# Performance work log

Hardware: AMD Instinct MI355X
Metric: run time of the kernel (lower is better)

The kernel has to match this reference:

```python
import jax, jax.numpy as jnp
import numpy as np

VOCAB = 50257
N_EMBD = 640
BLOCK = 256
B = 16


def setup_inputs() -> dict:
    key = jax.random.key(0)
    ks = jax.random.split(key, 8)
    std = 0.02
    return {
        "idx": jax.random.randint(ks[0], (B, BLOCK), 0, VOCAB, dtype=jnp.int64 if jax.config.jax_enable_x64 else jnp.int32),
        "w_embed": jax.random.normal(ks[1], (VOCAB, N_EMBD), jnp.float32) * std,
        "w_pos": jax.random.normal(ks[2], (BLOCK, N_EMBD), jnp.float32) * std,
        "wq": jax.random.normal(ks[3], (N_EMBD, N_EMBD), jnp.float32) * std,
        "wk": jax.random.normal(ks[4], (N_EMBD, N_EMBD), jnp.float32) * std,
        "wv": jax.random.normal(ks[5], (N_EMBD, N_EMBD), jnp.float32) * std,
        "w_out": jax.random.normal(ks[6], (VOCAB, N_EMBD), jnp.float32) * std,
        "b_out": jnp.zeros((VOCAB,), jnp.float32),
    }


def reference(idx, w_embed, w_pos, wq, wk, wv, w_out, b_out):
    # idx: (B, T) token ids. Dropout is identity (eval mode).
    Bt, T = idx.shape
    x = w_embed[idx] + w_pos[:T]                      # (B, T, D)
    q = jnp.einsum('btd,ed->bte', x, wq)              # torch Linear: x @ W.T
    k = jnp.einsum('btd,ed->bte', x, wk)
    v = jnp.einsum('btd,ed->bte', x, wv)
    scale = jnp.asarray(N_EMBD ** 0.5, x.dtype)
    scores = jnp.einsum('btd,bsd->bts', q, k) / scale  # (B, T, T)
    causal = jnp.triu(jnp.ones((T, T), bool), k=1)     # True above diagonal
    scores = jnp.where(causal, jnp.asarray(-jnp.inf, scores.dtype), scores)
    attn = jax.nn.softmax(scores, axis=-1)
    attn_out = jnp.einsum('bts,bsd->btd', attn, v)     # (B, T, D)
    logits = jnp.einsum('btd,vd->btv', attn_out, w_out) + b_out  # (B, T, V)
    return logits
```

## Files before the change

### kernel.cpp

```cpp
#include <hip/hip_runtime.h>
#include <hip/hip_bf16.h>
#include <stdint.h>

#define VOCAB 50257
#define VPAD  50304
#define DIM   640
#define SEQ   256
#define NBATCH 16
#define MROWS 4096

using bf16 = __hip_bfloat16;
typedef __attribute__((ext_vector_type(8))) short short8;
typedef __attribute__((ext_vector_type(4))) float f32x4;

__device__ __forceinline__ void gld_lds16(const void* g, void* l) {
  __builtin_amdgcn_global_load_lds(
      (const __attribute__((address_space(1))) void*)g,
      (__attribute__((address_space(3))) void*)l, 16, 0, 0);
}

__global__ void embed_kernel(const int* __restrict__ idx,
                             const float* __restrict__ we,
                             const float* __restrict__ wp,
                             bf16* __restrict__ xb) {
  int row = blockIdx.x;
  int t = row & (SEQ - 1);
  int tok = idx[row];
  const float* src = we + (long)tok * DIM;
  const float* pos = wp + (long)t * DIM;
  for (int d = threadIdx.x; d < DIM; d += blockDim.x)
    xb[(long)row * DIM + d] = __float2bfloat16(src[d] + pos[d]);
}

__global__ void conv_kernel(const float* __restrict__ src, bf16* __restrict__ dst,
                            long n_src, long n_dst) {
  long i = (long)blockIdx.x * blockDim.x + threadIdx.x;
  long stride = (long)gridDim.x * blockDim.x;
  for (; i < n_dst; i += stride)
    dst[i] = __float2bfloat16(i < n_src ? src[i] : 0.f);
}

__global__ void transpose_v(const bf16* __restrict__ v, bf16* __restrict__ vt) {
  long i = (long)blockIdx.x * blockDim.x + threadIdx.x;
  if (i >= (long)NBATCH * DIM * SEQ) return;
  int t = (int)(i & (SEQ - 1));
  long be = i >> 8;
  int e = (int)(be % DIM);
  int b = (int)(be / DIM);
  vt[i] = v[((long)b * SEQ + t) * DIM + e];
}

__global__ void softmax_kernel(const float* __restrict__ sc, bf16* __restrict__ p) {
  int wid = threadIdx.x >> 6, lane = threadIdx.x & 63;
  int row = blockIdx.x * 4 + wid;
  int t = row & (SEQ - 1);
  const float* srow = sc + (long)row * SEQ;
  const float rsc = 0.03952847075210474f;
  float v[4];
  float mx = -1e30f;
#pragma unroll
  for (int i = 0; i < 4; ++i) {
    int s = lane + 64 * i;
    v[i] = (s <= t) ? srow[s] * rsc : -1e30f;
    mx = fmaxf(mx, v[i]);
  }
#pragma unroll
  for (int off = 32; off; off >>= 1) mx = fmaxf(mx, __shfl_xor(mx, off, 64));
  float sum = 0.f;
#pragma unroll
  for (int i = 0; i < 4; ++i) {
    int s = lane + 64 * i;
    v[i] = (s <= t) ? __expf(v[i] - mx) : 0.f;
    sum += v[i];
  }
#pragma unroll
  for (int off = 32; off; off >>= 1) sum += __shfl_xor(sum, off, 64);
  float inv = 1.f / sum;
#pragma unroll
  for (int i = 0; i < 4; ++i)
    p[(long)row * SEQ + lane + 64 * i] = __float2bfloat16(v[i] * inv);
}

template <typename OUT_T, bool BIAS>
__global__ __launch_bounds__(256, 2) void gemm_bt(
    const bf16* __restrict__ Ag, const bf16* __restrict__ Bg,
    OUT_T* __restrict__ Cg, const float* __restrict__ bias,
    int K, int ldc, int Nstore, long sA, long sB, long sC) {
  __shared__ bf16 As[128 * 32];
  __shared__ bf16 Bs[128 * 32];
  const int tid = threadIdx.x;
  const int wv = tid >> 6, lane = tid & 63;
  const int tm = blockIdx.x * 128, tn = blockIdx.y * 128;
  const int bz = blockIdx.z;
  const bf16* A = Ag + (long)bz * sA + (long)tm * K;
  const bf16* B = Bg + (long)bz * sB + (long)tn * K;

  f32x4 acc[4][4] = {};
  const int wr = (wv >> 1) * 64, wc = (wv & 1) * 64;
  const int lr = lane & 15, lk = (lane >> 4) * 8;
  const int srow0 = wv * 32;
  const int g_r = lane >> 2, g_k = (lane & 3) * 8;

  for (int k0 = 0; k0 < K; k0 += 32) {
#pragma unroll
    for (int j = 0; j < 2; ++j) {
      int r = srow0 + j * 16;
      gld_lds16(A + (long)(r + g_r) * K + k0 + g_k, &As[r * 32]);
      gld_lds16(B + (long)(r + g_r) * K + k0 + g_k, &Bs[r * 32]);
    }
    __syncthreads();
    short8 a[4], b[4];
#pragma unroll
    for (int m = 0; m < 4; ++m)
      a[m] = *(const short8*)&As[(wr + m * 16 + lr) * 32 + lk];
#pragma unroll
    for (int n = 0; n < 4; ++n)
      b[n] = *(const short8*)&Bs[(wc + n * 16 + lr) * 32 + lk];
#pragma unroll
    for (int m = 0; m < 4; ++m)
#pragma unroll
      for (int n = 0; n < 4; ++n)
        acc[m][n] = __builtin_amdgcn_mfma_f32_16x16x32_bf16(a[m], b[n], acc[m][n], 0, 0, 0);
    __syncthreads();
  }

  OUT_T* C = Cg + (long)bz * sC;
  const int crow0 = tm + wr + (lane >> 4) * 4;
  const int ccol0 = tn + wc + (lane & 15);
#pragma unroll
  for (int m = 0; m < 4; ++m)
#pragma unroll
    for (int n = 0; n < 4; ++n) {
      int col = ccol0 + n * 16;
      if (col < Nstore) {
        float bv = BIAS ? bias[col] : 0.f;
#pragma unroll
        for (int j = 0; j < 4; ++j) {
          long row = crow0 + m * 16 + j;
          float val = acc[m][n][j] + bv;
          if constexpr (sizeof(OUT_T) == 2)
            C[row * ldc + col] = __float2bfloat16(val);
          else
            C[row * ldc + col] = val;
        }
      }
    }
}

extern "C" void kernel_launch(void* const* d_in, const int* in_sizes, int n_in,
                              void* d_out, int out_size, void* d_ws, size_t ws_size,
                              hipStream_t stream) {
  const int*   idx     = (const int*)d_in[0];
  const float* w_embed = (const float*)d_in[1];
  const float* w_pos   = (const float*)d_in[2];
  const float* wq      = (const float*)d_in[3];
  const float* wk      = (const float*)d_in[4];
  const float* wv      = (const float*)d_in[5];
  const float* w_out   = (const float*)d_in[6];
  const float* b_out   = (const float*)d_in[7];
  float* out = (float*)d_out;

  size_t off = 0;
  auto alloc = [&](size_t bytes) {
    void* p = (char*)d_ws + off;
    off += (bytes + 255) & ~(size_t)255;
    return p;
  };
  bf16* x_bf    = (bf16*)alloc((size_t)MROWS * DIM * 2);
  bf16* wqkv_bf = (bf16*)alloc((size_t)3 * DIM * DIM * 2);
  bf16* wout_bf = (bf16*)alloc((size_t)VPAD * DIM * 2);
  bf16* qkv     = (bf16*)alloc((size_t)3 * MROWS * DIM * 2);
  bf16* vT      = (bf16*)alloc((size_t)NBATCH * DIM * SEQ * 2);
  float* scores = (float*)alloc((size_t)NBATCH * SEQ * SEQ * 4);
  bf16* P       = (bf16*)alloc((size_t)NBATCH * SEQ * SEQ * 2);
  bf16* attn    = (bf16*)alloc((size_t)MROWS * DIM * 2);

  const long QKV_S = (long)MROWS * DIM;
  const long W_S   = (long)DIM * DIM;

  embed_kernel<<<MROWS, 256, 0, stream>>>(idx, w_embed, w_pos, x_bf);

  conv_kernel<<<512, 256, 0, stream>>>(wq, wqkv_bf,           W_S, W_S);
  conv_kernel<<<512, 256, 0, stream>>>(wk, wqkv_bf + W_S,     W_S, W_S);
  conv_kernel<<<512, 256, 0, stream>>>(wv, wqkv_bf + 2 * W_S, W_S, W_S);
  conv_kernel<<<4096, 256, 0, stream>>>(w_out, wout_bf, (long)VOCAB * DIM, (long)VPAD * DIM);

  gemm_bt<bf16, false><<<dim3(MROWS / 128, DIM / 128, 3), 256, 0, stream>>>(
      x_bf, wqkv_bf, qkv, nullptr, DIM, DIM, DIM, 0, W_S, QKV_S);

  {
    long n = (long)NBATCH * DIM * SEQ;
    transpose_v<<<(int)((n + 255) / 256), 256, 0, stream>>>(qkv + 2 * QKV_S, vT);
  }

  gemm_bt<float, false><<<dim3(SEQ / 128, SEQ / 128, NBATCH), 256, 0, stream>>>(
      qkv, qkv + QKV_S, scores, nullptr, DIM, SEQ, SEQ,
      (long)SEQ * DIM, (long)SEQ * DIM, (long)SEQ * SEQ);

  softmax_kernel<<<MROWS / 4, 256, 0, stream>>>(scores, P);

  gemm_bt<bf16, false><<<dim3(SEQ / 128, DIM / 128, NBATCH), 256, 0, stream>>>(
      P, vT, attn, nullptr, SEQ, DIM, DIM,
      (long)SEQ * SEQ, (long)DIM * SEQ, (long)SEQ * DIM);

  gemm_bt<float, true><<<dim3(MROWS / 128, VPAD / 128, 1), 256, 0, stream>>>(
      attn, wout_bf, out, b_out, DIM, VOCAB, VOCAB, 0, 0, 0);
}
```

Baseline: 625.9 us.

## Replace vocab projection GEMM with 256x256 double-buffered swizzled LDS kernel

```diff
diff --git a/kernel.cpp b/kernel.cpp
--- a/kernel.cpp
+++ b/kernel.cpp
@@ -3,11 +3,12 @@
 #include <stdint.h>
 
 #define VOCAB 50257
-#define VPAD  50304
+#define VPAD  50432
 #define DIM   640
 #define SEQ   256
 #define NBATCH 16
 #define MROWS 4096
+#define NTILES 10
 
 using bf16 = __hip_bfloat16;
 typedef __attribute__((ext_vector_type(8))) short short8;
@@ -18,6 +19,9 @@
       (const __attribute__((address_space(1))) void*)g,
       (__attribute__((address_space(3))) void*)l, 16, 0, 0);
 }
+
+#define BAR() asm volatile("s_barrier" ::: "memory")
+#define VMC(n) asm volatile("s_waitcnt vmcnt(" #n ")" ::: "memory")
 
 __global__ void embed_kernel(const int* __restrict__ idx,
                              const float* __restrict__ we,
@@ -143,6 +147,122 @@
           else
             C[row * ldc + col] = val;
         }
+      }
+    }
+}
+
+__global__ __launch_bounds__(512, 1) void gemm256(
+    const bf16* __restrict__ Ag, const bf16* __restrict__ Bg,
+    float* __restrict__ Cg, const float* __restrict__ bias) {
+  __shared__ __align__(16) char lds[131072];
+  const int tid = threadIdx.x;
+  const int lane = tid & 63, wv = tid >> 6;
+  const int wm = wv >> 2, wn = wv & 3;
+
+  int bid = blockIdx.x;
+  int swz = (bid & 7) * 394 + (bid >> 3);
+  const int tm = swz & 15, tn = swz >> 4;
+
+  int e0, e1, du0, du1;
+  {
+    int L0 = tid * 16;
+    int L1 = (512 + tid) * 16;
+    int Lp0 = L0 ^ (((L0 >> 9) & 1) << 5);
+    int Lp1 = L1 ^ (((L1 >> 9) & 1) << 5);
+    e0 = ((Lp0 >> 6) & 127) * DIM + ((Lp0 >> 13) & 1) * 32 + ((Lp0 & 63) >> 1);
+    e1 = ((Lp1 >> 6) & 127) * DIM + ((Lp1 >> 13) & 1) * 32 + ((Lp1 & 63) >> 1);
+    du0 = (wv << 6) * 16;
+    du1 = (512 + (wv << 6)) * 16;
+  }
+  auto STAGE = [&](int halfBase, const bf16* src) {
+    gld_lds16(src + e0, lds + halfBase + du0);
+    gld_lds16(src + e1, lds + halfBase + du1);
+  };
+
+  const bf16* Abase = Ag + (long)tm * 256 * DIM;
+  const bf16* Bbase = Bg + (long)tn * 256 * DIM;
+
+  const int lr = lane & 15, h16 = lane >> 4;
+  const int laneOff = (lr * 64 + h16 * 16) ^ ((lr & 8) << 2);
+  const int abase = wm * 16384 + laneOff;
+  const int bbase = 32768 + (wn >> 1) * 16384 + (wn & 1) * 4096 + laneOff;
+
+  f32x4 acc[8][4] = {};
+  short8 a0[2][4], a1[2][4], b[2][4];
+
+#define READ_A(DST, SLOT, MFB)                                                \
+  { _Pragma("unroll") for (int ks = 0; ks < 2; ++ks)                          \
+    _Pragma("unroll") for (int mf = 0; mf < 4; ++mf)                          \
+      DST[ks][mf] = *(const short8*)(lds + (SLOT) + abase + ks * 8192 +       \
+                                     ((MFB) + mf) * 1024); }
+#define READ_B(SLOT)                                                          \
+  { _Pragma("unroll") for (int ks = 0; ks < 2; ++ks)                          \
+    _Pragma("unroll") for (int nf = 0; nf < 4; ++nf)                          \
+      b[ks][nf] = *(const short8*)(lds + (SLOT) + bbase + ks * 8192 +         \
+                                   nf * 1024); }
+#define MFMA_G(AARR, KS, ROFF)                                                \
+  __builtin_amdgcn_s_setprio(1);                                              \
+  { _Pragma("unroll") for (int mf = 0; mf < 4; ++mf)                          \
+    _Pragma("unroll") for (int nf = 0; nf < 4; ++nf)                          \
+      acc[(ROFF) + mf][nf] = __builtin_amdgcn_mfma_f32_16x16x32_bf16(         \
+          AARR[KS][mf], b[KS][nf], acc[(ROFF) + mf][nf], 0, 0, 0); }          \
+  __builtin_amdgcn_s_setprio(0);
+
+  STAGE(0,             Abase);
+  STAGE(16384,         Abase + 128 * DIM);
+  STAGE(32768,         Bbase);
+  STAGE(49152,         Bbase + 128 * DIM);
+  STAGE(65536 + 32768, Bbase + 64);
+  STAGE(65536 + 0,     Abase + 64);
+  STAGE(65536 + 16384, Abase + 128 * DIM + 64);
+  VMC(6);
+  BAR();
+
+#pragma unroll
+  for (int T = 0; T < NTILES; ++T) {
+    const int slot = (T & 1) << 16;
+    const int nslot = ((T + 1) & 1) << 16;
+    READ_A(a0, slot, 0);
+    READ_B(slot);
+    if (T + 1 < NTILES) STAGE(nslot + 49152, Bbase + 128 * DIM + (T + 1) * 64);
+    BAR();
+    MFMA_G(a0, 0, 0);
+    BAR();
+    READ_A(a1, slot, 4);
+    if (T + 2 < NTILES) STAGE(slot + 32768, Bbase + (T + 2) * 64);
+    BAR();
+    MFMA_G(a0, 1, 0);
+    BAR();
+    if (T + 2 < NTILES) STAGE(slot + 0, Abase + (T + 2) * 64);
+    BAR();
+    MFMA_G(a1, 0, 4);
+    BAR();
+    if (T + 2 < NTILES) {
+      STAGE(slot + 16384, Abase + 128 * DIM + (T + 2) * 64);
+      VMC(6);
+    } else if (T + 1 < NTILES) {
+      VMC(0);
+    }
+    BAR();
+    MFMA_G(a1, 1, 4);
+    BAR();
+  }
+#undef READ_A
+#undef READ_B
+#undef MFMA_G
+
+  const int rowB = tm * 256 + wm * 128 + h16 * 4;
+  const int colB = tn * 256 + wn * 64 + lr;
+#pragma unroll
+  for (int mf = 0; mf < 8; ++mf)
+#pragma unroll
+    for (int nf = 0; nf < 4; ++nf) {
+      int col = colB + nf * 16;
+      if (col < VOCAB) {
+        float bv = bias[col];
+#pragma unroll
+        for (int jj = 0; jj < 4; ++jj)
+          Cg[(long)(rowB + mf * 16 + jj) * VOCAB + col] = acc[mf][nf][jj] + bv;
       }
     }
 }
@@ -203,6 +323,5 @@
       P, vT, attn, nullptr, SEQ, DIM, DIM,
       (long)SEQ * SEQ, (long)DIM * SEQ, (long)SEQ * DIM);
 
-  gemm_bt<float, true><<<dim3(MROWS / 128, VPAD / 128, 1), 256, 0, stream>>>(
-      attn, wout_bf, out, b_out, DIM, VOCAB, VOCAB, 0, 0, 0);
-}
+  gemm256<<<16 * 197, 512, 0, stream>>>(attn, wout_bf, out, b_out);
+}
```

New measurement: 652.5 us. 4.3% more time.

## Triple-buffer GEMM with swizzled LDS, XCD-aware tile remap, vectorized conversions

Applied to the files above, without the earlier changes.

```diff
diff --git a/kernel.cpp b/kernel.cpp
--- a/kernel.cpp
+++ b/kernel.cpp
@@ -3,7 +3,7 @@
 #include <stdint.h>
 
 #define VOCAB 50257
-#define VPAD  50304
+#define VPAD  50432
 #define DIM   640
 #define SEQ   256
 #define NBATCH 16
@@ -12,12 +12,16 @@
 using bf16 = __hip_bfloat16;
 typedef __attribute__((ext_vector_type(8))) short short8;
 typedef __attribute__((ext_vector_type(4))) float f32x4;
+struct bf16x4 { bf16 a, b, c, d; };
 
 __device__ __forceinline__ void gld_lds16(const void* g, void* l) {
   __builtin_amdgcn_global_load_lds(
       (const __attribute__((address_space(1))) void*)g,
       (__attribute__((address_space(3))) void*)l, 16, 0, 0);
 }
+
+#define BAR() asm volatile("s_barrier" ::: "memory")
+#define VMC(n) asm volatile("s_waitcnt vmcnt(" #n ")" ::: "memory")
 
 __global__ void embed_kernel(const int* __restrict__ idx,
                              const float* __restrict__ we,
@@ -28,16 +32,25 @@
   int tok = idx[row];
   const float* src = we + (long)tok * DIM;
   const float* pos = wp + (long)t * DIM;
-  for (int d = threadIdx.x; d < DIM; d += blockDim.x)
-    xb[(long)row * DIM + d] = __float2bfloat16(src[d] + pos[d]);
-}
-
-__global__ void conv_kernel(const float* __restrict__ src, bf16* __restrict__ dst,
-                            long n_src, long n_dst) {
-  long i = (long)blockIdx.x * blockDim.x + threadIdx.x;
-  long stride = (long)gridDim.x * blockDim.x;
-  for (; i < n_dst; i += stride)
-    dst[i] = __float2bfloat16(i < n_src ? src[i] : 0.f);
+  for (int d = threadIdx.x * 4; d < DIM; d += blockDim.x * 4) {
+    float4 s = *(const float4*)(src + d);
+    float4 p = *(const float4*)(pos + d);
+    bf16x4 o = { __float2bfloat16(s.x + p.x), __float2bfloat16(s.y + p.y),
+                 __float2bfloat16(s.z + p.z), __float2bfloat16(s.w + p.w) };
+    *(bf16x4*)(xb + (long)row * DIM + d) = o;
+  }
+}
+
+__global__ void conv4_kernel(const float* __restrict__ src, bf16* __restrict__ dst,
+                             long n_src, long n_dst) {
+  long i = ((long)blockIdx.x * blockDim.x + threadIdx.x) * 4;
+  long stride = (long)gridDim.x * blockDim.x * 4;
+  for (; i < n_dst; i += stride) {
+    float4 v = (i < n_src) ? *(const float4*)(src + i) : make_float4(0.f, 0.f, 0.f, 0.f);
+    bf16x4 o = { __float2bfloat16(v.x), __float2bfloat16(v.y),
+                 __float2bfloat16(v.z), __float2bfloat16(v.w) };
+    *(bf16x4*)(dst + i) = o;
+  }
 }
 
 __global__ void transpose_v(const bf16* __restrict__ v, bf16* __restrict__ vt) {
@@ -81,52 +94,86 @@
     p[(long)row * SEQ + lane + 64 * i] = __float2bfloat16(v[i] * inv);
 }
 
-template <typename OUT_T, bool BIAS>
-__global__ __launch_bounds__(256, 2) void gemm_bt(
+template <int NT, typename OUT_T, bool BIAS, bool SWZ>
+__global__ __launch_bounds__(256, 3) void gemm_pipe(
     const bf16* __restrict__ Ag, const bf16* __restrict__ Bg,
     OUT_T* __restrict__ Cg, const float* __restrict__ bias,
-    int K, int ldc, int Nstore, long sA, long sB, long sC) {
-  __shared__ bf16 As[128 * 32];
-  __shared__ bf16 Bs[128 * 32];
+    int K, int ldc, int Nstore, long sA, long sB, long sC,
+    int tmW, int chunk) {
+  __shared__ __align__(16) char lds[49152];
   const int tid = threadIdx.x;
-  const int wv = tid >> 6, lane = tid & 63;
-  const int tm = blockIdx.x * 128, tn = blockIdx.y * 128;
-  const int bz = blockIdx.z;
-  const bf16* A = Ag + (long)bz * sA + (long)tm * K;
-  const bf16* B = Bg + (long)bz * sB + (long)tn * K;
+  const int lane = tid & 63, wv = tid >> 6;
+  const int lr = lane & 15, h16 = lane >> 4;
+
+  int tm, tn, bz;
+  if constexpr (SWZ) {
+    int bid = blockIdx.x;
+    int s = (bid & 7) * chunk + (bid >> 3);
+    tm = s % tmW; tn = s / tmW; bz = 0;
+  } else {
+    tm = blockIdx.x; tn = blockIdx.y; bz = blockIdx.z;
+  }
+
+  const bf16* A = Ag + (long)bz * sA + (long)tm * 128 * K;
+  const bf16* B = Bg + (long)bz * sB + (long)tn * 128 * K;
+
+  int srcE[2], dstW[2];
+#pragma unroll
+  for (int j = 0; j < 2; ++j) {
+    int d = j * 256 + tid;
+    int b = d ^ ((d >> 3) & 3);
+    srcE[j] = (b >> 2) * K + (b & 3) * 8;
+    dstW[j] = (j * 256 + wv * 64) * 16;
+  }
+  auto STAGE = [&](int slot, int kOff) {
+#pragma unroll
+    for (int j = 0; j < 2; ++j) {
+      gld_lds16(A + srcE[j] + kOff, lds + slot + dstW[j]);
+      gld_lds16(B + srcE[j] + kOff, lds + slot + 8192 + dstW[j]);
+    }
+  };
+
+  const int wr = (wv >> 1) * 64, wc = (wv & 1) * 64;
+  int aoff[4], boff[4];
+#pragma unroll
+  for (int m = 0; m < 4; ++m) {
+    int La = (wr + m * 16 + lr) * 64 + h16 * 16;
+    aoff[m] = La ^ (((La >> 7) & 3) << 4);
+    int Lb = (wc + m * 16 + lr) * 64 + h16 * 16;
+    boff[m] = 8192 + (Lb ^ (((Lb >> 7) & 3) << 4));
+  }
 
   f32x4 acc[4][4] = {};
-  const int wr = (wv >> 1) * 64, wc = (wv & 1) * 64;
-  const int lr = lane & 15, lk = (lane >> 4) * 8;
-  const int srow0 = wv * 32;
-  const int g_r = lane >> 2, g_k = (lane & 3) * 8;
-
-  for (int k0 = 0; k0 < K; k0 += 32) {
-#pragma unroll
-    for (int j = 0; j < 2; ++j) {
-      int r = srow0 + j * 16;
-      gld_lds16(A + (long)(r + g_r) * K + k0 + g_k, &As[r * 32]);
-      gld_lds16(B + (long)(r + g_r) * K + k0 + g_k, &Bs[r * 32]);
-    }
-    __syncthreads();
-    short8 a[4], b[4];
-#pragma unroll
-    for (int m = 0; m < 4; ++m)
-      a[m] = *(const short8*)&As[(wr + m * 16 + lr) * 32 + lk];
-#pragma unroll
-    for (int n = 0; n < 4; ++n)
-      b[n] = *(const short8*)&Bs[(wc + n * 16 + lr) * 32 + lk];
+  short8 a[4], b[4];
+
+  STAGE(0, 0);
+  if (NT > 1) STAGE(16384, 32);
+  VMC(4);
+  BAR();
+
+#pragma unroll
+  for (int t = 0; t < NT; ++t) {
+    const int cur = (t % 3) * 16384;
+    if (t + 2 < NT) STAGE(((t + 2) % 3) * 16384, (t + 2) * 32);
+#pragma unroll
+    for (int m = 0; m < 4; ++m) a[m] = *(const short8*)(lds + cur + aoff[m]);
+#pragma unroll
+    for (int n = 0; n < 4; ++n) b[n] = *(const short8*)(lds + cur + boff[n]);
+    __builtin_amdgcn_s_setprio(1);
 #pragma unroll
     for (int m = 0; m < 4; ++m)
 #pragma unroll
       for (int n = 0; n < 4; ++n)
         acc[m][n] = __builtin_amdgcn_mfma_f32_16x16x32_bf16(a[m], b[n], acc[m][n], 0, 0, 0);
-    __syncthreads();
+    __builtin_amdgcn_s_setprio(0);
+    if (t + 2 < NT) { VMC(4); }
+    else if (t + 1 < NT) { VMC(0); }
+    BAR();
   }
 
   OUT_T* C = Cg + (long)bz * sC;
-  const int crow0 = tm + wr + (lane >> 4) * 4;
-  const int ccol0 = tn + wc + (lane & 15);
+  const int crow0 = tm * 128 + wr + h16 * 4;
+  const int ccol0 = tn * 128 + wc + lr;
 #pragma unroll
   for (int m = 0; m < 4; ++m)
 #pragma unroll
@@ -180,29 +227,29 @@
 
   embed_kernel<<<MROWS, 256, 0, stream>>>(idx, w_embed, w_pos, x_bf);
 
-  conv_kernel<<<512, 256, 0, stream>>>(wq, wqkv_bf,           W_S, W_S);
-  conv_kernel<<<512, 256, 0, stream>>>(wk, wqkv_bf + W_S,     W_S, W_S);
-  conv_kernel<<<512, 256, 0, stream>>>(wv, wqkv_bf + 2 * W_S, W_S, W_S);
-  conv_kernel<<<4096, 256, 0, stream>>>(w_out, wout_bf, (long)VOCAB * DIM, (long)VPAD * DIM);
-
-  gemm_bt<bf16, false><<<dim3(MROWS / 128, DIM / 128, 3), 256, 0, stream>>>(
-      x_bf, wqkv_bf, qkv, nullptr, DIM, DIM, DIM, 0, W_S, QKV_S);
+  conv4_kernel<<<256, 256, 0, stream>>>(wq, wqkv_bf,           W_S, W_S);
+  conv4_kernel<<<256, 256, 0, stream>>>(wk, wqkv_bf + W_S,     W_S, W_S);
+  conv4_kernel<<<256, 256, 0, stream>>>(wv, wqkv_bf + 2 * W_S, W_S, W_S);
+  conv4_kernel<<<2048, 256, 0, stream>>>(w_out, wout_bf, (long)VOCAB * DIM, (long)VPAD * DIM);
+
+  gemm_pipe<20, bf16, false, false><<<dim3(MROWS / 128, DIM / 128, 3), 256, 0, stream>>>(
+      x_bf, wqkv_bf, qkv, nullptr, DIM, DIM, DIM, 0, W_S, QKV_S, 0, 0);
 
   {
     long n = (long)NBATCH * DIM * SEQ;
     transpose_v<<<(int)((n + 255) / 256), 256, 0, stream>>>(qkv + 2 * QKV_S, vT);
   }
 
-  gemm_bt<float, false><<<dim3(SEQ / 128, SEQ / 128, NBATCH), 256, 0, stream>>>(
+  gemm_pipe<20, float, false, false><<<dim3(SEQ / 128, SEQ / 128, NBATCH), 256, 0, stream>>>(
       qkv, qkv + QKV_S, scores, nullptr, DIM, SEQ, SEQ,
-      (long)SEQ * DIM, (long)SEQ * DIM, (long)SEQ * SEQ);
+      (long)SEQ * DIM, (long)SEQ * DIM, (long)SEQ * SEQ, 0, 0);
 
   softmax_kernel<<<MROWS / 4, 256, 0, stream>>>(scores, P);
 
-  gemm_bt<bf16, false><<<dim3(SEQ / 128, DIM / 128, NBATCH), 256, 0, stream>>>(
+  gemm_pipe<8, bf16, false, false><<<dim3(SEQ / 128, DIM / 128, NBATCH), 256, 0, stream>>>(
       P, vT, attn, nullptr, SEQ, DIM, DIM,
-      (long)SEQ * SEQ, (long)DIM * SEQ, (long)SEQ * DIM);
-
-  gemm_bt<float, true><<<dim3(MROWS / 128, VPAD / 128, 1), 256, 0, stream>>>(
-      attn, wout_bf, out, b_out, DIM, VOCAB, VOCAB, 0, 0, 0);
-}
+      (long)SEQ * SEQ, (long)DIM * SEQ, (long)SEQ * DIM, 0, 0);
+
+  gemm_pipe<20, float, true, true><<<12608, 256, 0, stream>>>(
+      attn, wout_bf, out, b_out, DIM, VOCAB, VOCAB, 0, 0, 0, 32, 1576);
+}
```

New measurement: 742.0 us. +18.6%, slower.
